# Performance work log

Hardware: AMD Instinct MI355X
Metric: run time of the kernel (lower is better)

The kernel has to match this reference:

```python
import jax, jax.numpy as jnp
import numpy as np

EMB = 1024
HEADS = 8
NUM_REL = 5
BS = 8
SLEN = 1024


def setup_inputs() -> dict:
    key = jax.random.key(0)
    ks = jax.random.split(key, 11)

    def lin(k, out_dim, in_dim):
        k1, k2 = jax.random.split(k)
        w = 0.02 * jax.random.normal(k1, (out_dim, in_dim), dtype=jnp.float32)
        b = 0.02 * jax.random.normal(k2, (out_dim,), dtype=jnp.float32)
        return w, b

    p = {}
    for i, pref in enumerate(["nq", "nk", "nv", "no", "tq", "tk", "tv", "to"]):
        w, b = lin(ks[i], EMB, EMB)
        p[pref + "_w"] = w
        p[pref + "_b"] = b
    tp_w, tp_b = lin(ks[8], NUM_REL, EMB)
    h_in = jax.random.normal(ks[9], (BS, SLEN, EMB), dtype=jnp.float32)
    word_mask = jnp.ones((BS, SLEN), dtype=bool)
    return {"h_in": h_in, "word_mask": word_mask, **p, "tp_w": tp_w, "tp_b": tp_b}


def _mha(x, mask, qw, qb, kw, kb, vw, vb, ow, ob):
    # Self-attention with key-padding mask; returns (output, attn_weights).
    bs, slen, dim = x.shape
    dh = dim // HEADS

    def split(t):  # [bs, slen, dim] -> [bs, h, slen, dh]
        return t.reshape(bs, slen, HEADS, dh).transpose(0, 2, 1, 3)

    q = split(x @ qw.T + qb) / jnp.sqrt(jnp.asarray(dh, x.dtype))
    k = split(x @ kw.T + kb)
    v = split(x @ vw.T + vb)
    scores = jnp.einsum('bhqd,bhkd->bhqk', q, k)
    scores = jnp.where(mask[:, None, None, :], scores, jnp.asarray(-1e9, x.dtype))
    w = jax.nn.softmax(scores, axis=-1)  # [bs, h, slen, slen]
    ctx = jnp.einsum('bhqk,bhkd->bhqd', w, v).transpose(0, 2, 1, 3).reshape(bs, slen, dim)
    return ctx @ ow.T + ob, w


def reference(h_in, word_mask, nq_w, nq_b, nk_w, nk_b, nv_w, nv_b, no_w, no_b,
              tq_w, tq_b, tk_w, tk_b, tv_w, tv_b, to_w, to_b, tp_w, tp_b):
    # Edge norms: sum attention weights over heads, then symmetrize.
    _, norm_w = _mha(h_in, word_mask, nq_w, nq_b, nk_w, nk_b, nv_w, nv_b, no_w, no_b)
    norm_w = norm_w.sum(axis=1)  # edge_norm_agg == 'sum' -> [bs, slen, slen]
    norms = norm_w + norm_w.transpose(0, 2, 1)

    # Edge types: second attention, project to relation logits, pairwise outer-sum.
    type_out, _ = _mha(h_in, word_mask, tq_w, tq_b, tk_w, tk_b, tv_w, tv_b, to_w, to_b)
    logits = type_out @ tp_w.T + tp_b  # [bs, slen, R]
    pair = logits[:, :, None, :] + logits[:, None, :, :]  # [bs, slen, slen, R]
    type_probs = jax.nn.softmax(pair, axis=-1)  # log_softmax(...).exp()
    return norms, type_probs
```

## Files before the change

kernel.cpp:

```cpp
#include <hip/hip_runtime.h>

using u16 = unsigned short;
typedef __bf16 bf16x8 __attribute__((ext_vector_type(8)));
typedef float  f32x4  __attribute__((ext_vector_type(4)));

__device__ __forceinline__ float b2f(u16 u){
  union { unsigned int i; float f; } v; v.i = ((unsigned int)u) << 16; return v.f;
}
__device__ __forceinline__ u16 f2b(float f){
  union { float f; unsigned int i; } v; v.f = f;
  unsigned int r = v.i + 0x7FFFu + ((v.i >> 16) & 1u);
  return (u16)(r >> 16);
}
__device__ __forceinline__ float waveMax(float v){
  #pragma unroll
  for (int o = 32; o > 0; o >>= 1) v = fmaxf(v, __shfl_xor(v, o, 64));
  return v;
}
__device__ __forceinline__ float waveSum(float v){
  #pragma unroll
  for (int o = 32; o > 0; o >>= 1) v += __shfl_xor(v, o, 64);
  return v;
}
__device__ __forceinline__ void async_cp16(const u16* g, u16* l){
  __builtin_amdgcn_global_load_lds((const __attribute__((address_space(1))) void*)g,
                                   (__attribute__((address_space(3))) void*)l, 16, 0, 0);
}

__global__ __launch_bounds__(256)
void cvt_f2b4(const float* __restrict__ s, u16* __restrict__ d, long long n4)
{
  long long i = (long long)blockIdx.x * 256 + threadIdx.x;
  long long st = (long long)gridDim.x * 256;
  for (; i < n4; i += st) {
    float4 v = ((const float4*)s)[i];
    ushort4 o; o.x = f2b(v.x); o.y = f2b(v.y); o.z = f2b(v.z); o.w = f2b(v.w);
    ((ushort4*)d)[i] = o;
  }
}

__global__ __launch_bounds__(256)
void bcat_k(const float* b0, const float* b1, const float* b2, const float* b3,
            float* __restrict__ dst)
{
  int t = blockIdx.x * 256 + threadIdx.x;
  const float* s = (t < 1024) ? b0 : (t < 2048) ? b1 : (t < 3072) ? b2 : b3;
  dst[t] = s[t & 1023];
}

__global__ __launch_bounds__(256)
void fuse_w(const float* __restrict__ tow, const float* __restrict__ tob,
            const float* __restrict__ tpw, const float* __restrict__ tpb,
            float* __restrict__ Wc, float* __restrict__ bc)
{
  int t = blockIdx.x * 256 + threadIdx.x;
  int r = t >> 10, c = t & 1023;
  float acc = 0.f;
  for (int k = 0; k < 1024; k++) acc += tpw[r * 1024 + k] * tow[k * 1024 + c];
  Wc[t] = acc;
  if (t < 5) {
    float a = 0.f;
    for (int k = 0; k < 1024; k++) a += tpw[t * 1024 + k] * tob[k];
    bc[t] = a + tpb[t];
  }
}

__global__ __launch_bounds__(256)
void fuse_wf(const float* __restrict__ tvw, const float* __restrict__ tvb,
             const float* __restrict__ Wc, u16* __restrict__ WF,
             float* __restrict__ bias5)
{
  int idx = blockIdx.x * 256 + threadIdx.x;
  int n = idx >> 10, k = idx & 1023;
  float acc = 0.f;
  if (n < 40) {
    int h = n / 5, r = n - h * 5;
    const float* wcr = Wc + r * 1024 + h * 128;
    const float* tw = tvw + (h * 128) * 1024 + k;
    for (int d = 0; d < 128; d++) acc += wcr[d] * tw[d * 1024];
  }
  WF[idx] = f2b(acc);
  if (k == 0) {
    float a = 0.f;
    if (n < 40) {
      int h = n / 5, r = n - h * 5;
      for (int d = 0; d < 128; d++) a += Wc[r * 1024 + h * 128 + d] * tvb[h * 128 + d];
    }
    bias5[n] = a;
  }
}

template<int HAS_BIAS, int OUT_F32>
__global__ __launch_bounds__(256)
void gemm_bt(const u16* __restrict__ A, const u16* __restrict__ B,
             u16* __restrict__ C, const float* __restrict__ bias,
             int lda, int ldb, int ldc, int K,
             long long sAo, long long sAi, long long sBo, long long sBi,
             long long sCo, long long sCi, int zshift, int zmask, float alpha)
{
  int zo = (int)(blockIdx.z >> zshift), zi = (int)(blockIdx.z & zmask);
  A += zo * sAo + zi * sAi;
  B += zo * sBo + zi * sBi;
  long long coff = zo * sCo + zi * sCi;
  int m0 = blockIdx.y * 128, n0 = blockIdx.x * 128;

  __shared__ alignas(16) u16 sA[128 * 32];
  __shared__ alignas(16) u16 sB[128 * 32];

  int t = threadIdx.x;
  int lane = t & 63, wave = t >> 6;
  int quad = lane >> 4, l16 = lane & 15;
  int wm = (wave >> 1) << 6, wn = (wave & 1) << 6;
  int srow = t >> 2, scg = (t & 3) << 3;
  int wb = wave << 9;

  const u16* ga = A + (long long)(m0 + srow) * lda + scg;
  const u16* gb = B + (long long)(n0 + srow) * ldb + scg;

  f32x4 acc[4][4] = {};

  for (int k0 = 0; k0 < K; k0 += 32) {
    __syncthreads();
    async_cp16(ga + k0,                sA + wb);
    async_cp16(ga + 64ll * lda + k0,   sA + wb + 2048);
    async_cp16(gb + k0,                sB + wb);
    async_cp16(gb + 64ll * ldb + k0,   sB + wb + 2048);
    __syncthreads();

    bf16x8 af[4], bfr[4];
    #pragma unroll
    for (int mi = 0; mi < 4; mi++)
      af[mi] = *(const bf16x8*)(&sA[(wm + mi * 16 + l16) * 32 + quad * 8]);
    #pragma unroll
    for (int ni = 0; ni < 4; ni++)
      bfr[ni] = *(const bf16x8*)(&sB[(wn + ni * 16 + l16) * 32 + quad * 8]);
    #pragma unroll
    for (int mi = 0; mi < 4; mi++)
      #pragma unroll
      for (int ni = 0; ni < 4; ni++)
        acc[mi][ni] = __builtin_amdgcn_mfma_f32_16x16x32_bf16(af[mi], bfr[ni], acc[mi][ni], 0, 0, 0);
  }

  #pragma unroll
  for (int ni = 0; ni < 4; ni++) {
    int n = n0 + wn + ni * 16 + l16;
    float bv = 0.f;
    if (HAS_BIAS) bv = bias[n];
    #pragma unroll
    for (int mi = 0; mi < 4; mi++) {
      int mb = m0 + wm + mi * 16 + quad * 4;
      #pragma unroll
      for (int r = 0; r < 4; r++) {
        float v = alpha * (acc[mi][ni][r] + bv);
        if (OUT_F32) ((float*)C)[coff + (long long)(mb + r) * ldc + n] = v;
        else         C[coff + (long long)(mb + r) * ldc + n] = f2b(v);
      }
    }
  }
}

__global__ __launch_bounds__(512)
void norm_fused(const u16* __restrict__ proj, float* __restrict__ out)
{
  int b = blockIdx.y, i0 = blockIdx.x * 32;
  int t = threadIdx.x;
  int lane = t & 63, wave = t >> 6;
  int quad = lane >> 4, l16 = lane & 15;
  int wm = (wave >> 2) << 4;
  int wn = (wave & 3) << 4;
  int r0 = t >> 4, g = t & 15;

  __shared__ alignas(16) u16 sQ[2][32 * 128];
  __shared__ alignas(16) u16 sK[2][64 * 128];
  __shared__ alignas(16) u16 sS[32 * 1044];

  const long long ldp = 4096;
  const u16* pb = proj + (long long)(b * 1024) * ldp;
  int srow = t >> 4;
  int scol = (t & 15) << 3;
  const float qs = 0.08838834764831845f;

  float acc[16][4];
  #pragma unroll
  for (int k = 0; k < 16; k++)
    #pragma unroll
    for (int j = 0; j < 4; j++) acc[k][j] = 0.f;

  auto stageQ = [&](int h, int buf){
    async_cp16(pb + (long long)(i0 + srow) * ldp + h * 128 + scol,
               &sQ[buf][wave << 9]);
  };
  auto stageK = [&](int h, int jt, int buf){
    const u16* gbase = pb + 1024 + h * 128 + scol;
    #pragma unroll
    for (int c = 0; c < 2; c++)
      async_cp16(gbase + (long long)(jt * 64 + c * 32 + srow) * ldp,
                 &sK[buf][c * 4096 + (wave << 9)]);
  };

  int qb = 0, kb = 0;
  stageQ(0, 0);
  stageK(0, 0, 0);
  __syncthreads();

  for (int h = 0; h < 8; h++) {
    for (int jt = 0; jt < 16; jt++) {
      if (jt < 15)      stageK(h, jt + 1, kb ^ 1);
      else if (h < 7) { stageK(h + 1, 0, kb ^ 1); stageQ(h + 1, qb ^ 1); }

      f32x4 accs = {};
      #pragma unroll
      for (int kk = 0; kk < 4; kk++) {
        bf16x8 af  = *(const bf16x8*)(&sQ[qb][(wm + l16) * 128 + kk * 32 + quad * 8]);
        bf16x8 bf_ = *(const bf16x8*)(&sK[kb][(wn + l16) * 128 + kk * 32 + quad * 8]);
        accs = __builtin_amdgcn_mfma_f32_16x16x32_bf16(af, bf_, accs, 0, 0, 0);
      }
      int jg = jt * 64 + wn + l16;
      #pragma unroll
      for (int rr = 0; rr < 4; rr++)
        sS[(wm + quad * 4 + rr) * 1044 + jg] = f2b(qs * accs[rr]);
      __syncthreads();
      kb ^= 1;
    }

    const u16* sr = sS + r0 * 1044 + g * 4;
    float m = -1e30f;
    #pragma unroll
    for (int k = 0; k < 16; k++) {
      ushort4 u = *(const ushort4*)(sr + k * 64);
      m = fmaxf(m, fmaxf(fmaxf(b2f(u.x), b2f(u.y)), fmaxf(b2f(u.z), b2f(u.w))));
    }
    #pragma unroll
    for (int o = 1; o < 16; o <<= 1) m = fmaxf(m, __shfl_xor(m, o, 64));
    float s = 0.f;
    #pragma unroll
    for (int k = 0; k < 16; k++) {
      ushort4 u = *(const ushort4*)(sr + k * 64);
      s += __expf(b2f(u.x) - m) + __expf(b2f(u.y) - m)
         + __expf(b2f(u.z) - m) + __expf(b2f(u.w) - m);
    }
    #pragma unroll
    for (int o = 1; o < 16; o <<= 1) s += __shfl_xor(s, o, 64);
    float inv = 1.f / s;
    #pragma unroll
    for (int k = 0; k < 16; k++) {
      ushort4 u = *(const ushort4*)(sr + k * 64);
      acc[k][0] += __expf(b2f(u.x) - m) * inv;
      acc[k][1] += __expf(b2f(u.y) - m) * inv;
      acc[k][2] += __expf(b2f(u.z) - m) * inv;
      acc[k][3] += __expf(b2f(u.w) - m) * inv;
    }
    __syncthreads();
    qb ^= 1;
  }

  float* orow = out + ((long long)b << 20) + ((long long)(i0 + r0) << 10) + g * 4;
  #pragma unroll
  for (int k = 0; k < 16; k++) {
    float4 o4 = make_float4(acc[k][0], acc[k][1], acc[k][2], acc[k][3]);
    *(float4*)(orow + k * 64) = o4;
  }
}

__global__ __launch_bounds__(256)
void sym_inplace(float* __restrict__ nw)
{
  int tj = blockIdx.x, ti = blockIdx.y, b = blockIdx.z;
  if (tj < ti) return;
  float* base = nw + ((long long)b << 20);
  __shared__ float sij[64][65], sji[64][65];
  int t = threadIdx.x;
  #pragma unroll
  for (int p = 0; p < 16; p++) {
    int idx = p * 256 + t; int r = idx >> 6, c = idx & 63;
    sij[r][c] = base[(long long)(ti * 64 + r) * 1024 + tj * 64 + c];
    sji[r][c] = base[(long long)(tj * 64 + r) * 1024 + ti * 64 + c];
  }
  __syncthreads();
  #pragma unroll
  for (int p = 0; p < 16; p++) {
    int idx = p * 256 + t; int r = idx >> 6, c = idx & 63;
    base[(long long)(ti * 64 + r) * 1024 + tj * 64 + c] = sij[r][c] + sji[c][r];
    if (ti != tj)
      base[(long long)(tj * 64 + r) * 1024 + ti * 64 + c] = sji[r][c] + sij[c][r];
  }
}

__global__ __launch_bounds__(256)
void w5_tr(const float* __restrict__ w5b, float* __restrict__ w5)
{
  int bh = blockIdx.y, b = bh >> 3, h = bh & 7;
  int j = blockIdx.x * 256 + threadIdx.x;
  const float* src = w5b + (long long)(b * 1024 + j) * 128 + h * 5;
  float* dst = w5 + (long long)bh * 5120 + j;
  #pragma unroll
  for (int r = 0; r < 5; r++) dst[r * 1024] = src[r];
}

__global__ __launch_bounds__(256)
void type_logits(const u16* __restrict__ sc, const float* __restrict__ w5,
                 const float* __restrict__ bc, float* __restrict__ lg)
{
  int b = blockIdx.y;
  int t = threadIdx.x;
  int wave = t >> 6, l = t & 63;
  int i = blockIdx.x * 4 + wave;
  __shared__ float sW5[5120];
  float acc[5] = {0.f, 0.f, 0.f, 0.f, 0.f};

  for (int h = 0; h < 8; h++) {
    const u16* row = sc + (((long long)(b * 8 + h)) << 20) + ((long long)i << 10);
    const float* wb = w5 + ((long long)(b * 8 + h)) * 5120;
    float v[16];
    #pragma unroll
    for (int k = 0; k < 16; k++) v[k] = b2f(row[l + 64 * k]);
    __syncthreads();
    #pragma unroll
    for (int p = 0; p < 20; p++) sW5[p * 256 + t] = wb[p * 256 + t];
    float m = v[0];
    #pragma unroll
    for (int k = 1; k < 16; k++) m = fmaxf(m, v[k]);
    m = waveMax(m);
    float e[16], s = 0.f;
    #pragma unroll
    for (int k = 0; k < 16; k++) { e[k] = __expf(v[k] - m); s += e[k]; }
    s = waveSum(s);
    float inv = 1.f / s;
    __syncthreads();
    #pragma unroll
    for (int r = 0; r < 5; r++) {
      float a = 0.f;
      #pragma unroll
      for (int k = 0; k < 16; k++) a += e[k] * sW5[r * 1024 + l + 64 * k];
      acc[r] += a * inv;
    }
  }
  #pragma unroll
  for (int r = 0; r < 5; r++) acc[r] = waveSum(acc[r]);
  if (l == 0) {
    #pragma unroll
    for (int r = 0; r < 5; r++) lg[(long long)(b * 1024 + i) * 5 + r] = acc[r] + bc[r];
  }
}

__global__ __launch_bounds__(256)
void pairwise_probs(const float* __restrict__ lg, float* __restrict__ out)
{
  int i = blockIdx.x, b = blockIdx.y;
  int t = threadIdx.x;
  __shared__ float sin_[5120];
  __shared__ float sout[5120];
  const float* lb = lg + (long long)b * 5120;
  #pragma unroll
  for (int p = 0; p < 20; p++) sin_[p * 256 + t] = lb[p * 256 + t];
  __syncthreads();
  float li[5];
  #pragma unroll
  for (int r = 0; r < 5; r++) li[r] = sin_[i * 5 + r];
  #pragma unroll
  for (int p = 0; p < 4; p++) {
    int j = t + 256 * p;
    float x[5]; float m = -1e30f;
    #pragma unroll
    for (int r = 0; r < 5; r++) { x[r] = li[r] + sin_[j * 5 + r]; m = fmaxf(m, x[r]); }
    float s = 0.f;
    #pragma unroll
    for (int r = 0; r < 5; r++) { x[r] = __expf(x[r] - m); s += x[r]; }
    float inv = 1.f / s;
    #pragma unroll
    for (int r = 0; r < 5; r++) sout[j * 5 + r] = x[r] * inv;
  }
  __syncthreads();
  float4* ob = (float4*)(out + ((long long)(b * 1024 + i)) * 5120);
  #pragma unroll
  for (int q = 0; q < 5; q++) ob[q * 256 + t] = ((const float4*)sout)[q * 256 + t];
}

extern "C" void kernel_launch(void* const* d_in, const int* in_sizes, int n_in,
                              void* d_out, int out_size, void* d_ws, size_t ws_size,
                              hipStream_t stream)
{
  const float* h_in = (const float*)d_in[0];
  const float* nq_w = (const float*)d_in[2];
  const float* nq_b = (const float*)d_in[3];
  const float* nk_w = (const float*)d_in[4];
  const float* nk_b = (const float*)d_in[5];
  const float* tq_w = (const float*)d_in[10];
  const float* tq_b = (const float*)d_in[11];
  const float* tk_w = (const float*)d_in[12];
  const float* tk_b = (const float*)d_in[13];
  const float* tv_w = (const float*)d_in[14];
  const float* tv_b = (const float*)d_in[15];
  const float* to_w = (const float*)d_in[16];
  const float* to_b = (const float*)d_in[17];
  const float* tp_w = (const float*)d_in[18];
  const float* tp_b = (const float*)d_in[19];

  char* ws = (char*)d_ws;
  u16*   hb    = (u16*)(ws);
  u16*   wcat  = (u16*)(ws + (16ll << 20));
  float* bcat  = (float*)(ws + (24ll << 20));
  float* Wc    = (float*)(ws + (24ll << 20) + (64 << 10));
  float* bc    = (float*)(ws + (24ll << 20) + (128 << 10));
  float* bias5 = (float*)(ws + (24ll << 20) + (192 << 10));
  u16*   WF    = (u16*)(ws + (24ll << 20) + (256 << 10));
  float* lg    = (float*)(ws + (25ll << 20));
  float* w5b   = (float*)(ws + (26ll << 20));
  float* w5    = (float*)(ws + (30ll << 20));
  u16*   proj  = (u16*)(ws + (32ll << 20));
  u16*   sc    = (u16*)(ws + (96ll << 20));

  float* out_norms = (float*)d_out;
  float* out_types = (float*)d_out + 8388608ll;

  const float qs = 0.08838834764831845f;
  dim3 blk(256);

  cvt_f2b4<<<dim3(2048), blk, 0, stream>>>(h_in, hb, 2097152ll);
  cvt_f2b4<<<dim3(512),  blk, 0, stream>>>(nq_w, wcat,              262144ll);
  cvt_f2b4<<<dim3(512),  blk, 0, stream>>>(nk_w, wcat + 1048576ll,  262144ll);
  cvt_f2b4<<<dim3(512),  blk, 0, stream>>>(tq_w, wcat + 2097152ll,  262144ll);
  cvt_f2b4<<<dim3(512),  blk, 0, stream>>>(tk_w, wcat + 3145728ll,  262144ll);
  bcat_k<<<dim3(16), blk, 0, stream>>>(nq_b, nk_b, tq_b, tk_b, bcat);
  fuse_w<<<dim3(20), blk, 0, stream>>>(to_w, to_b, tp_w, tp_b, Wc, bc);
  fuse_wf<<<dim3(512), blk, 0, stream>>>(tv_w, tv_b, Wc, WF, bias5);

  gemm_bt<1,0><<<dim3(32,64,1), blk, 0, stream>>>(hb, wcat, proj, bcat,
      1024,1024,4096,1024, 0,0,0,0,0,0, 0,0, 1.f);

  gemm_bt<1,1><<<dim3(1,64,1), blk, 0, stream>>>(hb, WF, (u16*)w5b, bias5,
      1024,1024,128,1024, 0,0,0,0,0,0, 0,0, 1.f);
  w5_tr<<<dim3(4,64), blk, 0, stream>>>(w5b, w5);

  norm_fused<<<dim3(32,8), dim3(512), 0, stream>>>(proj, out_norms);
  sym_inplace<<<dim3(16,16,8), blk, 0, stream>>>(out_norms);

  gemm_bt<0,0><<<dim3(8,8,64), blk, 0, stream>>>(proj + 2048, proj + 3072, sc, nullptr,
      4096,4096,1024,128, 4194304ll,128ll, 4194304ll,128ll, 8388608ll,1048576ll, 3,7, qs);
  type_logits<<<dim3(256,8), blk, 0, stream>>>(sc, w5, bc, lg);
  pairwise_probs<<<dim3(1024,8), blk, 0, stream>>>(lg, out_types);
}
```

Measured before the change: 789.5 us.

## Swap fused paths: flash-style type attention, materialized scores for norm branch

The type branch now runs a flash-style kernel: it computes Q·K scores with MFMA per head and folds them into an online softmax against the five fused weights, writing per-head partial logits. A small reduction kernel then sums the heads. This avoids writing and rereading the full bf16 score tensor for that branch. The norm branch goes the other way: its score tensor is written out by the batched GEMM and a simple per-row softmax-sum kernel reads it back. The net effect on memory traffic and parallelism depends on the balance between the two branches.

```diff
diff --git a/kernel.cpp b/kernel.cpp
--- a/kernel.cpp
+++ b/kernel.cpp
@@ -159,107 +159,39 @@
   }
 }
 
-__global__ __launch_bounds__(512)
-void norm_fused(const u16* __restrict__ proj, float* __restrict__ out)
-{
-  int b = blockIdx.y, i0 = blockIdx.x * 32;
+__global__ __launch_bounds__(256)
+void norm_softmax_sum(const u16* __restrict__ sc, float* __restrict__ out)
+{
+  int i = blockIdx.x, b = blockIdx.y;
   int t = threadIdx.x;
-  int lane = t & 63, wave = t >> 6;
-  int quad = lane >> 4, l16 = lane & 15;
-  int wm = (wave >> 2) << 4;
-  int wn = (wave & 3) << 4;
-  int r0 = t >> 4, g = t & 15;
-
-  __shared__ alignas(16) u16 sQ[2][32 * 128];
-  __shared__ alignas(16) u16 sK[2][64 * 128];
-  __shared__ alignas(16) u16 sS[32 * 1044];
-
-  const long long ldp = 4096;
-  const u16* pb = proj + (long long)(b * 1024) * ldp;
-  int srow = t >> 4;
-  int scol = (t & 15) << 3;
-  const float qs = 0.08838834764831845f;
-
-  float acc[16][4];
-  #pragma unroll
-  for (int k = 0; k < 16; k++)
-    #pragma unroll
-    for (int j = 0; j < 4; j++) acc[k][j] = 0.f;
-
-  auto stageQ = [&](int h, int buf){
-    async_cp16(pb + (long long)(i0 + srow) * ldp + h * 128 + scol,
-               &sQ[buf][wave << 9]);
-  };
-  auto stageK = [&](int h, int jt, int buf){
-    const u16* gbase = pb + 1024 + h * 128 + scol;
-    #pragma unroll
-    for (int c = 0; c < 2; c++)
-      async_cp16(gbase + (long long)(jt * 64 + c * 32 + srow) * ldp,
-                 &sK[buf][c * 4096 + (wave << 9)]);
-  };
-
-  int qb = 0, kb = 0;
-  stageQ(0, 0);
-  stageK(0, 0, 0);
-  __syncthreads();
+  int wave = t >> 6;
+  __shared__ float wm_[4], wsu[4];
+  float acc[4] = {0.f, 0.f, 0.f, 0.f};
 
   for (int h = 0; h < 8; h++) {
-    for (int jt = 0; jt < 16; jt++) {
-      if (jt < 15)      stageK(h, jt + 1, kb ^ 1);
-      else if (h < 7) { stageK(h + 1, 0, kb ^ 1); stageQ(h + 1, qb ^ 1); }
-
-      f32x4 accs = {};
-      #pragma unroll
-      for (int kk = 0; kk < 4; kk++) {
-        bf16x8 af  = *(const bf16x8*)(&sQ[qb][(wm + l16) * 128 + kk * 32 + quad * 8]);
-        bf16x8 bf_ = *(const bf16x8*)(&sK[kb][(wn + l16) * 128 + kk * 32 + quad * 8]);
-        accs = __builtin_amdgcn_mfma_f32_16x16x32_bf16(af, bf_, accs, 0, 0, 0);
-      }
-      int jg = jt * 64 + wn + l16;
-      #pragma unroll
-      for (int rr = 0; rr < 4; rr++)
-        sS[(wm + quad * 4 + rr) * 1044 + jg] = f2b(qs * accs[rr]);
-      __syncthreads();
-      kb ^= 1;
-    }
-
-    const u16* sr = sS + r0 * 1044 + g * 4;
-    float m = -1e30f;
-    #pragma unroll
-    for (int k = 0; k < 16; k++) {
-      ushort4 u = *(const ushort4*)(sr + k * 64);
-      m = fmaxf(m, fmaxf(fmaxf(b2f(u.x), b2f(u.y)), fmaxf(b2f(u.z), b2f(u.w))));
-    }
-    #pragma unroll
-    for (int o = 1; o < 16; o <<= 1) m = fmaxf(m, __shfl_xor(m, o, 64));
-    float s = 0.f;
-    #pragma unroll
-    for (int k = 0; k < 16; k++) {
-      ushort4 u = *(const ushort4*)(sr + k * 64);
-      s += __expf(b2f(u.x) - m) + __expf(b2f(u.y) - m)
-         + __expf(b2f(u.z) - m) + __expf(b2f(u.w) - m);
-    }
-    #pragma unroll
-    for (int o = 1; o < 16; o <<= 1) s += __shfl_xor(s, o, 64);
+    const u16* row = sc + (((long long)(b * 8 + h)) << 20) + ((long long)i << 10);
+    float v[4];
+    #pragma unroll
+    for (int p = 0; p < 4; p++) v[p] = b2f(row[t + 256 * p]);
+    float m = fmaxf(fmaxf(v[0], v[1]), fmaxf(v[2], v[3]));
+    m = waveMax(m);
+    if ((t & 63) == 0) wm_[wave] = m;
+    __syncthreads();
+    m = fmaxf(fmaxf(wm_[0], wm_[1]), fmaxf(wm_[2], wm_[3]));
+    float e[4], s = 0.f;
+    #pragma unroll
+    for (int p = 0; p < 4; p++) { e[p] = __expf(v[p] - m); s += e[p]; }
+    s = waveSum(s);
+    if ((t & 63) == 0) wsu[wave] = s;
+    __syncthreads();
+    s = wsu[0] + wsu[1] + wsu[2] + wsu[3];
     float inv = 1.f / s;
     #pragma unroll
-    for (int k = 0; k < 16; k++) {
-      ushort4 u = *(const ushort4*)(sr + k * 64);
-      acc[k][0] += __expf(b2f(u.x) - m) * inv;
-      acc[k][1] += __expf(b2f(u.y) - m) * inv;
-      acc[k][2] += __expf(b2f(u.z) - m) * inv;
-      acc[k][3] += __expf(b2f(u.w) - m) * inv;
-    }
-    __syncthreads();
-    qb ^= 1;
-  }
-
-  float* orow = out + ((long long)b << 20) + ((long long)(i0 + r0) << 10) + g * 4;
-  #pragma unroll
-  for (int k = 0; k < 16; k++) {
-    float4 o4 = make_float4(acc[k][0], acc[k][1], acc[k][2], acc[k][3]);
-    *(float4*)(orow + k * 64) = o4;
-  }
+    for (int p = 0; p < 4; p++) acc[p] += e[p] * inv;
+  }
+  float* o = out + ((long long)b << 20) + ((long long)i << 10);
+  #pragma unroll
+  for (int p = 0; p < 4; p++) o[t + 256 * p] = acc[p];
 }
 
 __global__ __launch_bounds__(256)
@@ -298,49 +230,124 @@
 }
 
 __global__ __launch_bounds__(256)
-void type_logits(const u16* __restrict__ sc, const float* __restrict__ w5,
-                 const float* __restrict__ bc, float* __restrict__ lg)
-{
-  int b = blockIdx.y;
+void type_flash(const u16* __restrict__ proj, const float* __restrict__ w5,
+                float* __restrict__ plg)
+{
+  int i0 = blockIdx.x * 64, h = blockIdx.y, b = blockIdx.z;
   int t = threadIdx.x;
-  int wave = t >> 6, l = t & 63;
-  int i = blockIdx.x * 4 + wave;
+  int lane = t & 63, wave = t >> 6;
+  int quad = lane >> 4, l16 = lane & 15;
+
+  __shared__ alignas(16) u16 sK[2][64 * 128];
   __shared__ float sW5[5120];
-  float acc[5] = {0.f, 0.f, 0.f, 0.f, 0.f};
-
-  for (int h = 0; h < 8; h++) {
-    const u16* row = sc + (((long long)(b * 8 + h)) << 20) + ((long long)i << 10);
-    const float* wb = w5 + ((long long)(b * 8 + h)) * 5120;
-    float v[16];
-    #pragma unroll
-    for (int k = 0; k < 16; k++) v[k] = b2f(row[l + 64 * k]);
+
+  const u16* pb = proj + (long long)(b * 1024) * 4096;
+  const float qs = 0.08838834764831845f;
+
+  const float* wsrc = w5 + (long long)(b * 8 + h) * 5120;
+  #pragma unroll
+  for (int p = 0; p < 20; p++) sW5[p * 256 + t] = wsrc[p * 256 + t];
+
+  const u16* qrow = pb + (long long)(i0 + wave * 16 + l16) * 4096 + 2048 + h * 128 + quad * 8;
+  bf16x8 qf[4];
+  #pragma unroll
+  for (int kk = 0; kk < 4; kk++) qf[kk] = *(const bf16x8*)(qrow + kk * 32);
+
+  float m[4], ssum[4], acc5[4][5];
+  #pragma unroll
+  for (int r = 0; r < 4; r++) {
+    m[r] = -1e30f; ssum[r] = 0.f;
+    #pragma unroll
+    for (int c = 0; c < 5; c++) acc5[r][c] = 0.f;
+  }
+
+  auto stageK = [&](int step, int buf){
+    int j0 = step * 64;
+    #pragma unroll
+    for (int p = 0; p < 4; p++) {
+      int row = (p * 4 + wave) * 4 + (lane >> 4);
+      int u = lane & 15;
+      const u16* src = pb + (long long)(j0 + row) * 4096 + 3072 + h * 128
+                       + ((u ^ (row & 7)) << 3);
+      async_cp16(src, &sK[buf][(p * 4 + wave) * 512]);
+    }
+  };
+
+  stageK(0, 0);
+  __syncthreads();
+
+  int buf = 0;
+  for (int step = 0; step < 16; step++) {
+    if (step < 15) stageK(step + 1, buf ^ 1);
+    #pragma unroll
+    for (int sub = 0; sub < 4; sub++) {
+      int row = sub * 16 + l16;
+      f32x4 acc = {};
+      #pragma unroll
+      for (int kk = 0; kk < 4; kk++) {
+        bf16x8 bf_ = *(const bf16x8*)(&sK[buf][row * 128 + (((kk * 4 + quad) ^ (l16 & 7)) << 3)]);
+        acc = __builtin_amdgcn_mfma_f32_16x16x32_bf16(qf[kk], bf_, acc, 0, 0, 0);
+      }
+      int j = step * 64 + sub * 16 + l16;
+      float w0 = sW5[j], w1 = sW5[1024 + j], w2 = sW5[2048 + j],
+            w3 = sW5[3072 + j], w4 = sW5[4096 + j];
+      #pragma unroll
+      for (int r = 0; r < 4; r++) {
+        float sv = qs * acc[r];
+        if (sv > m[r] + 8.f) {
+          float f = __expf(m[r] - sv);
+          ssum[r] *= f;
+          #pragma unroll
+          for (int c = 0; c < 5; c++) acc5[r][c] *= f;
+          m[r] = sv;
+        }
+        float p_ = __expf(sv - m[r]);
+        ssum[r] += p_;
+        acc5[r][0] += p_ * w0; acc5[r][1] += p_ * w1; acc5[r][2] += p_ * w2;
+        acc5[r][3] += p_ * w3; acc5[r][4] += p_ * w4;
+      }
+    }
     __syncthreads();
-    #pragma unroll
-    for (int p = 0; p < 20; p++) sW5[p * 256 + t] = wb[p * 256 + t];
-    float m = v[0];
-    #pragma unroll
-    for (int k = 1; k < 16; k++) m = fmaxf(m, v[k]);
-    m = waveMax(m);
-    float e[16], s = 0.f;
-    #pragma unroll
-    for (int k = 0; k < 16; k++) { e[k] = __expf(v[k] - m); s += e[k]; }
-    s = waveSum(s);
+    buf ^= 1;
+  }
+
+  #pragma unroll
+  for (int r = 0; r < 4; r++) {
+    float M = m[r];
+    #pragma unroll
+    for (int o = 1; o < 16; o <<= 1) M = fmaxf(M, __shfl_xor(M, o, 64));
+    float f = __expf(m[r] - M);
+    float s = ssum[r] * f;
+    #pragma unroll
+    for (int o = 1; o < 16; o <<= 1) s += __shfl_xor(s, o, 64);
     float inv = 1.f / s;
-    __syncthreads();
-    #pragma unroll
-    for (int r = 0; r < 5; r++) {
-      float a = 0.f;
+    float outv = 0.f;
+    #pragma unroll
+    for (int c = 0; c < 5; c++) {
+      float a = acc5[r][c] * f;
       #pragma unroll
-      for (int k = 0; k < 16; k++) a += e[k] * sW5[r * 1024 + l + 64 * k];
-      acc[r] += a * inv;
-    }
-  }
-  #pragma unroll
-  for (int r = 0; r < 5; r++) acc[r] = waveSum(acc[r]);
-  if (l == 0) {
-    #pragma unroll
-    for (int r = 0; r < 5; r++) lg[(long long)(b * 1024 + i) * 5 + r] = acc[r] + bc[r];
-  }
+      for (int o = 1; o < 16; o <<= 1) a += __shfl_xor(a, o, 64);
+      outv = (l16 == c) ? a * inv : outv;
+    }
+    if (l16 < 5) {
+      int i = i0 + wave * 16 + quad * 4 + r;
+      plg[((long long)((b * 8 + h) * 1024 + i)) * 5 + l16] = outv;
+    }
+  }
+}
+
+__global__ __launch_bounds__(256)
+void lg_reduce(const float* __restrict__ plg, const float* __restrict__ bc,
+               float* __restrict__ lg)
+{
+  int idx = blockIdx.x * 256 + threadIdx.x;
+  int row = idx / 5, r = idx - row * 5;
+  int b = row >> 10, i = row & 1023;
+  float a = bc[r];
+  #pragma unroll
+  for (int h = 0; h < 8; h++)
+    a += plg[(((long long)((b * 8 + h) << 10)) + i) * 5 + r];
+  lg[idx] = a;
 }
 
 __global__ __launch_bounds__(256)
@@ -407,8 +414,9 @@
   float* lg    = (float*)(ws + (25ll << 20));
   float* w5b   = (float*)(ws + (26ll << 20));
   float* w5    = (float*)(ws + (30ll << 20));
-  u16*   proj  = (u16*)(ws + (32ll << 20));
-  u16*   sc    = (u16*)(ws + (96ll << 20));
+  float* plg   = (float*)(ws + (32ll << 20));
+  u16*   proj  = (u16*)(ws + (40ll << 20));
+  u16*   sc    = (u16*)(ws + (104ll << 20));
 
   float* out_norms = (float*)d_out;
   float* out_types = (float*)d_out + 8388608ll;
@@ -432,11 +440,12 @@
       1024,1024,128,1024, 0,0,0,0,0,0, 0,0, 1.f);
   w5_tr<<<dim3(4,64), blk, 0, stream>>>(w5b, w5);
 
-  norm_fused<<<dim3(32,8), dim3(512), 0, stream>>>(proj, out_norms);
+  gemm_bt<0,0><<<dim3(8,8,64), blk, 0, stream>>>(proj, proj + 1024, sc, nullptr,
+      4096,4096,1024,128, 4194304ll,128ll, 4194304ll,128ll, 8388608ll,1048576ll, 3,7, qs);
+  norm_softmax_sum<<<dim3(1024,8), blk, 0, stream>>>(sc, out_norms);
   sym_inplace<<<dim3(16,16,8), blk, 0, stream>>>(out_norms);
 
-  gemm_bt<0,0><<<dim3(8,8,64), blk, 0, stream>>>(proj + 2048, proj + 3072, sc, nullptr,
-      4096,4096,1024,128, 4194304ll,128ll, 4194304ll,128ll, 8388608ll,1048576ll, 3,7, qs);
-  type_logits<<<dim3(256,8), blk, 0, stream>>>(sc, w5, bc, lg);
+  type_flash<<<dim3(16,8,8), blk, 0, stream>>>(proj, w5, plg);
+  lg_reduce<<<dim3(160), blk, 0, stream>>>(plg, bc, lg);
   pairwise_probs<<<dim3(1024,8), blk, 0, stream>>>(lg, out_types);
 }
```

Result: faster. 682.1 us (-13.6%).
